# Kernel tuning notes

Hardware: AMD Instinct MI355X
Metric: run time of the kernel (lower is better)

Reference implementation:

```python
import jax, jax.numpy as jnp
import numpy as np

B, CLIP, P, E, H = 1024, 1024, 32, 2048, 16  # batch, clip_dim, prefix_length, token_emb_dim, num_heads
DH = E // H  # head dim = 128


def setup_inputs() -> dict:
    key = jax.random.key(0)
    ks = jax.random.split(key, 8)
    w = lambda k, sh: (jax.random.normal(k, sh, jnp.float32) * 0.02)
    return {
        "image_embs": jax.random.normal(ks[0], (B, CLIP), jnp.float32),
        "Wm": w(ks[1], (E, CLIP)),           # memory_proj weight
        "bm": jnp.zeros((E,), jnp.float32),
        "prefix_queries": w(ks[2], (P, E)),   # learned prefix queries
        "Win": w(ks[3], (3 * E, E)),          # MHA packed in_proj weight [q;k;v]
        "bin": jnp.zeros((3 * E,), jnp.float32),
        "Wo_mha": w(ks[4], (E, E)),           # MHA out_proj
        "bo_mha": jnp.zeros((E,), jnp.float32),
        "Wo": w(ks[5], (E, E)),               # adapter out_proj
        "bo": jnp.zeros((E,), jnp.float32),
    }


def reference(image_embs, Wm, bm, prefix_queries, Win, bin, Wo_mha, bo_mha, Wo, bo):
    Bn = image_embs.shape[0]
    # memory_proj: (B, clip_dim) -> (B, E); memory seq length is 1
    mem = image_embs @ Wm.T + bm
    # packed q/k/v projections, as in nn.MultiheadAttention
    Wq, Wk, Wv = Win[:E], Win[E:2 * E], Win[2 * E:]
    bq, bk, bv = bin[:E], bin[E:2 * E], bin[2 * E:]
    q = prefix_queries @ Wq.T + bq          # (P, E), shared across batch (queries are expanded)
    k = mem @ Wk.T + bk                     # (B, E)
    v = mem @ Wv.T + bv                     # (B, E)
    qh = q.reshape(P, H, DH)                # (P, H, dh)
    kh = k.reshape(Bn, H, DH)               # (B, H, dh)
    vh = v.reshape(Bn, H, DH)               # (B, H, dh)
    # scaled dot-product attention with kv_len = 1
    scores = jnp.einsum("phd,bhd->bhp", qh, kh) / jnp.sqrt(jnp.float32(DH))  # (B, H, P)
    attn = jax.nn.softmax(scores[..., None], axis=-1)  # (B, H, P, 1); trivially all-ones
    attn_out = jnp.einsum("bhpk,bhkd->bphd", attn, vh[:, :, None, :])  # (B, P, H, dh)
    attn_out = attn_out.reshape(Bn, P, E)
    out = attn_out @ Wo_mha.T + bo_mha      # MHA out_proj
    out = out @ Wo.T + bo                   # adapter out_proj
    return out
```

## Files before the change

### kernel.cpp

```cpp
#include <hip/hip_runtime.h>


#define BM 64
#define BN 64
#define BK 64
#define NBUF 5

typedef __attribute__((ext_vector_type(8))) __bf16 bf16x8;
typedef __attribute__((ext_vector_type(4))) float f32x4;

__device__ __forceinline__ unsigned short f2bf(float f) {
  unsigned int u = __float_as_uint(f);
  u += 0x7FFFu + ((u >> 16) & 1u);
  return (unsigned short)(u >> 16);
}

__device__ __forceinline__ void gload_lds16(const void* g, void* l) {
  __builtin_amdgcn_global_load_lds(
      (const __attribute__((address_space(1))) void*)g,
      (__attribute__((address_space(3))) void*)l, 16, 0, 0);
}

__global__ __launch_bounds__(256) void cvt_xw(const float* __restrict__ x,
                                              const float* __restrict__ wm,
                                              unsigned short* __restrict__ dst) {
  size_t i = (size_t)blockIdx.x * blockDim.x + threadIdx.x;
  for (; i < 786432; i += 262144) {
    const float4 v = (i < 262144)
        ? reinterpret_cast<const float4*>(x)[i]
        : reinterpret_cast<const float4*>(wm)[i - 262144];
    ushort4 o;
    o.x = f2bf(v.x); o.y = f2bf(v.y); o.z = f2bf(v.z); o.w = f2bf(v.w);
    reinterpret_cast<ushort4*>(dst)[i] = o;
  }
}

template <int EPI, bool CVT>
__global__ __launch_bounds__(256, 2) void gemm_bt(
    const unsigned short* __restrict__ A, const unsigned short* __restrict__ W,
    const float* __restrict__ bias, void* __restrict__ outp, int K,
    const float* __restrict__ cvt_src, unsigned short* __restrict__ cvt_dst,
    int cvt_n4) {
  __shared__ __attribute__((aligned(16))) unsigned short As[NBUF][BM * BK];
  __shared__ __attribute__((aligned(16))) unsigned short Bs[NBUF][BN * BK];
  const int tid = threadIdx.x;
  const int lane = tid & 63;
  const int wid = tid >> 6;
  const int rm = (wid >> 1) * 32;
  const int cn = (wid & 1) * 32;
  const int bid = blockIdx.x;
  const int bn0 = ((bid & 7) * 4 + (bid >> 7)) * BN;
  const int bm0 = ((bid >> 3) & 15) * BM;
  const int l15 = lane & 15;
  const int l4 = lane >> 4;
  const int lr = lane >> 3;
  const int lc = lane & 7;
  const int scol = ((lc ^ lr) << 3);
  const size_t Kz = (size_t)K;

  f32x4 acc[2][2] = {};

  auto stage = [&](int buf, int tile) {
    const int k0 = tile * BK;
#pragma unroll
    for (int j = 0; j < 2; ++j) {
      const int c = wid * 2 + j;
      gload_lds16(A + (size_t)(bm0 + c * 8 + lr) * Kz + (k0 + scol),
                  &As[buf][c * 512]);
      gload_lds16(W + (size_t)(bn0 + c * 8 + lr) * Kz + (k0 + scol),
                  &Bs[buf][c * 512]);
    }
  };

  auto compute = [&](int buf) {
    const int swz = (l15 & 7) << 3;
#pragma unroll
    for (int ks = 0; ks < 2; ++ks) {
      const int kidx = (ks * 32 + l4 * 8) ^ swz;
      bf16x8 a[2], b[2];
#pragma unroll
      for (int mi = 0; mi < 2; ++mi)
        a[mi] = *reinterpret_cast<const bf16x8*>(
            &As[buf][(rm + mi * 16 + l15) * 64 + kidx]);
#pragma unroll
      for (int ni = 0; ni < 2; ++ni)
        b[ni] = *reinterpret_cast<const bf16x8*>(
            &Bs[buf][(cn + ni * 16 + l15) * 64 + kidx]);
#pragma unroll
      for (int mi = 0; mi < 2; ++mi)
#pragma unroll
        for (int ni = 0; ni < 2; ++ni)
          acc[mi][ni] = __builtin_amdgcn_mfma_f32_16x16x32_bf16(
              a[mi], b[ni], acc[mi][ni], 0, 0, 0);
    }
  };

  const int nt = K >> 6;
  stage(0, 0); stage(1, 1); stage(2, 2); stage(3, 3);
  int b0 = 0, b1 = 1, b2 = 2, b3 = 3, b4 = 4;
  int t = 0;
  for (; t < nt - 4; ++t) {
    asm volatile("s_waitcnt vmcnt(12)" ::: "memory");
    asm volatile("s_waitcnt lgkmcnt(0)" ::: "memory");
    __builtin_amdgcn_s_barrier();
    stage(b4, t + 4);
    compute(b0);
    const int tmp = b0; b0 = b1; b1 = b2; b2 = b3; b3 = b4; b4 = tmp;
  }
  asm volatile("s_waitcnt vmcnt(12) lgkmcnt(0)" ::: "memory");
  __builtin_amdgcn_s_barrier();
  compute(b0);
  asm volatile("s_waitcnt vmcnt(8) lgkmcnt(0)" ::: "memory");
  __builtin_amdgcn_s_barrier();
  compute(b1);
  asm volatile("s_waitcnt vmcnt(4) lgkmcnt(0)" ::: "memory");
  __builtin_amdgcn_s_barrier();
  compute(b2);
  asm volatile("s_waitcnt vmcnt(0) lgkmcnt(0)" ::: "memory");
  __builtin_amdgcn_s_barrier();
  compute(b3);

  if (EPI == 0) {
#pragma unroll
    for (int mi = 0; mi < 2; ++mi)
#pragma unroll
      for (int ni = 0; ni < 2; ++ni) {
        const int col = bn0 + cn + ni * 16 + l15;
        const float bcol = bias[col];
#pragma unroll
        for (int i = 0; i < 4; ++i) {
          const int row = bm0 + rm + mi * 16 + l4 * 4 + i;
          ((unsigned short*)outp)[(size_t)row * 2048 + col] =
              f2bf(acc[mi][ni][i] + bcol);
        }
      }
  } else {
    asm volatile("s_waitcnt lgkmcnt(0)" ::: "memory");
    __builtin_amdgcn_s_barrier();
    float* Cs = (float*)As;
#pragma unroll
    for (int mi = 0; mi < 2; ++mi)
#pragma unroll
      for (int ni = 0; ni < 2; ++ni) {
        const int col = cn + ni * 16 + l15;
        const float bcol = bias[bn0 + col];
#pragma unroll
        for (int i = 0; i < 4; ++i)
          Cs[(rm + mi * 16 + l4 * 4 + i) * 68 + col] = acc[mi][ni][i] + bcol;
      }
    asm volatile("s_waitcnt lgkmcnt(0)" ::: "memory");
    __builtin_amdgcn_s_barrier();
    float* outf = (float*)outp;
    const int c4 = (lane & 15) * 4;
    const int psub = lane >> 4;
#pragma unroll
    for (int it = 0; it < 16; ++it) {
      const int rl = wid * 16 + it;
      const f32x4 v = *reinterpret_cast<const f32x4*>(&Cs[rl * 68 + c4]);
      float* ob = outf + ((size_t)(bm0 + rl) * 32 + psub) * 2048 + bn0 + c4;
#pragma unroll
      for (int pb = 0; pb < 8; ++pb)
        __builtin_nontemporal_store(
            v, reinterpret_cast<f32x4*>(ob + (size_t)pb * 4 * 2048));
    }
  }

  if (CVT) {
    size_t i = (size_t)bid * 256 + tid;
    for (; i < (size_t)cvt_n4; i += 131072) {
      const float4 v = reinterpret_cast<const float4*>(cvt_src)[i];
      ushort4 o;
      o.x = f2bf(v.x); o.y = f2bf(v.y); o.z = f2bf(v.z); o.w = f2bf(v.w);
      reinterpret_cast<ushort4*>(cvt_dst)[i] = o;
    }
  }
}

extern "C" void kernel_launch(void* const* d_in, const int* in_sizes, int n_in,
                              void* d_out, int out_size, void* d_ws, size_t ws_size,
                              hipStream_t stream) {
  const float* image = (const float*)d_in[0];
  const float* Wm   = (const float*)d_in[1];
  const float* bm   = (const float*)d_in[2];
  const float* Win  = (const float*)d_in[4];
  const float* bin  = (const float*)d_in[5];
  const float* Wo1  = (const float*)d_in[6];
  const float* bo1  = (const float*)d_in[7];
  const float* Wo2  = (const float*)d_in[8];
  const float* bo2  = (const float*)d_in[9];
  float* out = (float*)d_out;

  const float* Wv = Win + (size_t)2 * 2048 * 2048;
  const float* bv = bin + 2 * 2048;

  unsigned short* wsb = (unsigned short*)d_ws;
  unsigned short* Xb   = wsb;
  unsigned short* Wmb  = wsb + (1u << 20);
  unsigned short* Wvb  = wsb + (3u << 20);
  unsigned short* W1b  = wsb + (7u << 20);
  unsigned short* W2b  = wsb + (11u << 20);
  unsigned short* act0 = wsb + (15u << 20);
  unsigned short* act1 = wsb + (17u << 20);
  unsigned short* act2 = wsb + (19u << 20);

  cvt_xw<<<1024, 256, 0, stream>>>(image, Wm, wsb);

  gemm_bt<0, true><<<512, 256, 0, stream>>>(Xb, Wmb, bm, act0, 1024,
                                            Wv, Wvb, 1048576);
  gemm_bt<0, true><<<512, 256, 0, stream>>>(act0, Wvb, bv, act1, 2048,
                                            Wo1, W1b, 1048576);
  gemm_bt<0, true><<<512, 256, 0, stream>>>(act1, W1b, bo1, act2, 2048,
                                            Wo2, W2b, 1048576);
  gemm_bt<1, false><<<512, 256, 0, stream>>>(act2, W2b, bo2, out, 2048,
                                             nullptr, nullptr, 0);
  (void)n_in; (void)in_sizes; (void)out_size; (void)ws_size;
}
```

Measured before the change: 140.4 us.

## Halve GEMM K-tile to 32 with six-buffer pipeline and higher occupancy

Shrinks the K tile from 64 to 32 and grows the LDS ring from 5 to 6 buffers, which cuts shared memory per block so three blocks can fit per CU (launch bounds raised to 3). Each stage now issues one 16-byte async load per operand per thread, with a new XOR swizzle for the 32-wide rows. The next stage is issued before the wait/barrier instead of after it, so one more tile is in flight. The cost is twice as many barriers per K, each guarding only half the MFMA work, and tighter register limits that could cause spills.

```diff
diff --git a/kernel.cpp b/kernel.cpp
--- a/kernel.cpp
+++ b/kernel.cpp
@@ -3,8 +3,8 @@
 
 #define BM 64
 #define BN 64
-#define BK 64
-#define NBUF 5
+#define BK 32
+#define NBUF 6
 
 typedef __attribute__((ext_vector_type(8))) __bf16 bf16x8;
 typedef __attribute__((ext_vector_type(4))) float f32x4;
@@ -36,7 +36,7 @@
 }
 
 template <int EPI, bool CVT>
-__global__ __launch_bounds__(256, 2) void gemm_bt(
+__global__ __launch_bounds__(256, 3) void gemm_bt(
     const unsigned short* __restrict__ A, const unsigned short* __restrict__ W,
     const float* __restrict__ bias, void* __restrict__ outp, int K,
     const float* __restrict__ cvt_src, unsigned short* __restrict__ cvt_dst,
@@ -53,72 +53,65 @@
   const int bm0 = ((bid >> 3) & 15) * BM;
   const int l15 = lane & 15;
   const int l4 = lane >> 4;
-  const int lr = lane >> 3;
-  const int lc = lane & 7;
-  const int scol = ((lc ^ lr) << 3);
+  const int srow = lane >> 2;
+  const int sslot = (lane & 3) ^ ((lane >> 3) & 3);
   const size_t Kz = (size_t)K;
 
   f32x4 acc[2][2] = {};
 
   auto stage = [&](int buf, int tile) {
     const int k0 = tile * BK;
-#pragma unroll
-    for (int j = 0; j < 2; ++j) {
-      const int c = wid * 2 + j;
-      gload_lds16(A + (size_t)(bm0 + c * 8 + lr) * Kz + (k0 + scol),
-                  &As[buf][c * 512]);
-      gload_lds16(W + (size_t)(bn0 + c * 8 + lr) * Kz + (k0 + scol),
-                  &Bs[buf][c * 512]);
-    }
+    gload_lds16(A + (size_t)(bm0 + wid * 16 + srow) * Kz + (k0 + sslot * 8),
+                &As[buf][wid * 512]);
+    gload_lds16(W + (size_t)(bn0 + wid * 16 + srow) * Kz + (k0 + sslot * 8),
+                &Bs[buf][wid * 512]);
   };
 
   auto compute = [&](int buf) {
-    const int swz = (l15 & 7) << 3;
-#pragma unroll
-    for (int ks = 0; ks < 2; ++ks) {
-      const int kidx = (ks * 32 + l4 * 8) ^ swz;
-      bf16x8 a[2], b[2];
-#pragma unroll
-      for (int mi = 0; mi < 2; ++mi)
-        a[mi] = *reinterpret_cast<const bf16x8*>(
-            &As[buf][(rm + mi * 16 + l15) * 64 + kidx]);
+    const int rsw = (l15 >> 1) & 3;
+    const int kidx = (l4 ^ rsw) * 8;
+    bf16x8 a[2], b[2];
+#pragma unroll
+    for (int mi = 0; mi < 2; ++mi)
+      a[mi] = *reinterpret_cast<const bf16x8*>(
+          &As[buf][(rm + mi * 16 + l15) * BK + kidx]);
+#pragma unroll
+    for (int ni = 0; ni < 2; ++ni)
+      b[ni] = *reinterpret_cast<const bf16x8*>(
+          &Bs[buf][(cn + ni * 16 + l15) * BK + kidx]);
+#pragma unroll
+    for (int mi = 0; mi < 2; ++mi)
 #pragma unroll
       for (int ni = 0; ni < 2; ++ni)
-        b[ni] = *reinterpret_cast<const bf16x8*>(
-            &Bs[buf][(cn + ni * 16 + l15) * 64 + kidx]);
-#pragma unroll
-      for (int mi = 0; mi < 2; ++mi)
-#pragma unroll
-        for (int ni = 0; ni < 2; ++ni)
-          acc[mi][ni] = __builtin_amdgcn_mfma_f32_16x16x32_bf16(
-              a[mi], b[ni], acc[mi][ni], 0, 0, 0);
-    }
+        acc[mi][ni] = __builtin_amdgcn_mfma_f32_16x16x32_bf16(
+            a[mi], b[ni], acc[mi][ni], 0, 0, 0);
   };
 
-  const int nt = K >> 6;
+  const int nt = K >> 5;
   stage(0, 0); stage(1, 1); stage(2, 2); stage(3, 3);
-  int b0 = 0, b1 = 1, b2 = 2, b3 = 3, b4 = 4;
+  int cb = 0, sb = 4;
   int t = 0;
   for (; t < nt - 4; ++t) {
-    asm volatile("s_waitcnt vmcnt(12)" ::: "memory");
+    stage(sb, t + 4);
+    asm volatile("s_waitcnt vmcnt(8)" ::: "memory");
     asm volatile("s_waitcnt lgkmcnt(0)" ::: "memory");
     __builtin_amdgcn_s_barrier();
-    stage(b4, t + 4);
-    compute(b0);
-    const int tmp = b0; b0 = b1; b1 = b2; b2 = b3; b3 = b4; b4 = tmp;
-  }
-  asm volatile("s_waitcnt vmcnt(12) lgkmcnt(0)" ::: "memory");
-  __builtin_amdgcn_s_barrier();
-  compute(b0);
-  asm volatile("s_waitcnt vmcnt(8) lgkmcnt(0)" ::: "memory");
-  __builtin_amdgcn_s_barrier();
-  compute(b1);
+    compute(cb);
+    cb = (cb == NBUF - 1) ? 0 : cb + 1;
+    sb = (sb == NBUF - 1) ? 0 : sb + 1;
+  }
+  asm volatile("s_waitcnt vmcnt(6) lgkmcnt(0)" ::: "memory");
+  __builtin_amdgcn_s_barrier();
+  compute(cb); cb = (cb == NBUF - 1) ? 0 : cb + 1;
   asm volatile("s_waitcnt vmcnt(4) lgkmcnt(0)" ::: "memory");
   __builtin_amdgcn_s_barrier();
-  compute(b2);
+  compute(cb); cb = (cb == NBUF - 1) ? 0 : cb + 1;
+  asm volatile("s_waitcnt vmcnt(2) lgkmcnt(0)" ::: "memory");
+  __builtin_amdgcn_s_barrier();
+  compute(cb); cb = (cb == NBUF - 1) ? 0 : cb + 1;
   asm volatile("s_waitcnt vmcnt(0) lgkmcnt(0)" ::: "memory");
   __builtin_amdgcn_s_barrier();
-  compute(b3);
+  compute(cb);
 
   if (EPI == 0) {
 #pragma unroll
```

Result: slower. 145.3 us, median of 2 (+3.5%).
